# Optimization experiments

Hardware: AMD Instinct MI355X
Metric: run time of the kernel (lower is better)

Reference implementation:

```python
import jax, jax.numpy as jnp
import numpy as np
import math

B, P = 64, 2048
E_DRUG, E_PATH = 512, 512
ATTN_DIM, H, DEPTH = 1024, 8, 1
HD = ATTN_DIM // (2 * H)          # head_dim = 64
SCALING = HD ** (-0.5)
LAMBDA_INIT = 0.8 - 0.6 * math.exp(-0.3 * DEPTH)
EPS_SM = 1e-20
EPS_RMS = 1e-5


def stable_softmax(x, eps=EPS_SM):
    x = x.astype(jnp.float32)
    x = x - jnp.max(x, axis=-1, keepdims=True)
    ex = jnp.exp(x)
    return ex / (jnp.sum(ex, axis=-1, keepdims=True) + eps)


def setup_inputs() -> dict:
    key = jax.random.key(0)
    ks = jax.random.split(key, 11)
    d = 2 * H * HD  # = ATTN_DIM
    return {
        "query": jax.random.normal(ks[0], (B, 1, E_DRUG), jnp.float32),
        "key": jax.random.normal(ks[1], (B, P, E_PATH), jnp.float32),
        # Linear weights stored [in, out] (transpose of torch storage; same math)
        "Wq": jax.random.normal(ks[2], (E_DRUG, d), jnp.float32) * 0.02,
        "Wk": jax.random.normal(ks[3], (E_PATH, d), jnp.float32) * 0.02,
        "Wv": jax.random.normal(ks[4], (E_PATH, d), jnp.float32) * 0.02,
        "Wo": jax.random.normal(ks[5], (d, E_DRUG), jnp.float32) * 0.02,
        "lambda_q1": jax.random.normal(ks[6], (HD,), jnp.float32) * 0.1,
        "lambda_k1": jax.random.normal(ks[7], (HD,), jnp.float32) * 0.1,
        "lambda_q2": jax.random.normal(ks[8], (HD,), jnp.float32) * 0.1,
        "lambda_k2": jax.random.normal(ks[9], (HD,), jnp.float32) * 0.1,
        "rms_weight": jnp.ones((2 * HD,), jnp.float32),
    }


def reference(query, key, Wq, Wk, Wv, Wo,
              lambda_q1, lambda_k1, lambda_q2, lambda_k2, rms_weight):
    # Q: [B,1,H,2,HD] -> [B,H,2,1,HD]; K,V: [B,P,H,2,HD] -> [B,H,2,P,HD]
    Q = (query @ Wq).reshape(B, 1, H, 2, HD).transpose(0, 2, 3, 1, 4) * SCALING
    K = (key @ Wk).reshape(B, P, H, 2, HD).transpose(0, 2, 3, 1, 4)
    V = (key @ Wv).reshape(B, P, H, 2, HD)

    # scores: [B,H,2,1,P]
    scores = jnp.einsum('bhsqd,bhskd->bhsqk', Q, K)
    scores = stable_softmax(scores)

    lam1 = jnp.exp(jnp.sum(lambda_q1 * lambda_k1))
    lam2 = jnp.exp(jnp.sum(lambda_q2 * lambda_k2))
    lam = lam1 - lam2 + LAMBDA_INIT

    diff_attn = scores[:, :, 0] - lam * scores[:, :, 1]  # [B,H,1,P]

    V_cat = V.transpose(0, 2, 1, 3, 4).reshape(B, H, P, 2 * HD)  # [B,H,P,2HD]
    out = jnp.einsum('bhqp,bhpd->bhqd', diff_attn, V_cat)        # [B,H,1,2HD]

    # RMSNorm over last dim, affine
    var = jnp.mean(out * out, axis=-1, keepdims=True)
    out = out * jax.lax.rsqrt(var + EPS_RMS) * rms_weight
    out = out * (1.0 - LAMBDA_INIT)

    out = out.transpose(0, 2, 1, 3).reshape(B, 1, 2 * H * HD)
    out = out @ Wo  # [B,1,E_DRUG]
    return out, diff_attn
```

## Files before the change

### kernel.cpp

```cpp
#include <hip/hip_runtime.h>
#include <hip/hip_bf16.h>
#include <math.h>

#define B_ 64
#define P_ 2048
#define E_ 512
#define H_ 8
#define D_ 1024
#define NCH_ 16
#define NSC_ 64
#define NG_ 4
#define SMEM_FUSED (131072 + 4608 + 1280 + 64 + 64)

#define BAR() do { asm volatile("s_waitcnt lgkmcnt(0)" ::: "memory"); \
                   __builtin_amdgcn_s_barrier(); } while (0)
#define VM0() asm volatile("s_waitcnt vmcnt(0)" ::: "memory")

static constexpr float SCALING_C = 0.125f;
static constexpr float LAMBDA_INIT_C = 0.35550906759096966f;

typedef float f32x4 __attribute__((ext_vector_type(4)));
typedef float f32x2 __attribute__((ext_vector_type(2)));
typedef short bf16x8 __attribute__((ext_vector_type(8)));

static __device__ __forceinline__ short f2bf(float f) {
    unsigned u = __builtin_bit_cast(unsigned, f);
    unsigned r = (u + 0x7fffu + ((u >> 16) & 1u)) >> 16;
    return (short)r;
}

static __device__ __forceinline__ void gload_lds16(const float* g, char* l) {
    __builtin_amdgcn_global_load_lds(
        (const __attribute__((address_space(1))) void*)g,
        (__attribute__((address_space(3))) void*)l, 16, 0, 0);
}

__global__ __launch_bounds__(256) void k_qproj(const float* __restrict__ query,
                                               const float* __restrict__ Wq,
                                               const float* __restrict__ Wk,
                                               unsigned short* __restrict__ qkfrag) {
    int x = blockIdx.x, b = blockIdx.y, t = threadIdx.x;
    __shared__ float q[E_];
    __shared__ float qh[256];
    q[t] = query[b * E_ + t];
    q[t + 256] = query[b * E_ + t + 256];
    __syncthreads();
    {
        int j = x * 256 + t;
        const float* w = Wq + j;
        float s[8] = {0.f,0.f,0.f,0.f,0.f,0.f,0.f,0.f};
        #pragma unroll 4
        for (int e = 0; e < E_; e += 8) {
            #pragma unroll
            for (int k = 0; k < 8; ++k) s[k] += q[e + k] * w[(long)(e + k) * D_];
        }
        qh[t] = (((s[0]+s[1])+(s[2]+s[3])) + ((s[4]+s[5])+(s[6]+s[7]))) * SCALING_C;
    }
    __syncthreads();
    int hs_loc = t >> 6, l = t & 63;
    int hs = x * 4 + hs_loc;
    int e0 = l * 8;
    const float* qp = qh + hs_loc * 64;
    float acc[8];
    #pragma unroll
    for (int jj = 0; jj < 8; ++jj) {
        const f32x4* w = (const f32x4*)(Wk + (long)(e0 + jj) * D_ + hs * 64);
        float s = 0.f;
        #pragma unroll
        for (int d4 = 0; d4 < 16; ++d4) {
            f32x4 wv = w[d4];
            s += qp[d4 * 4 + 0] * wv[0] + qp[d4 * 4 + 1] * wv[1]
               + qp[d4 * 4 + 2] * wv[2] + qp[d4 * 4 + 3] * wv[3];
        }
        acc[jj] = s;
    }
    bf16x8 v;
    #pragma unroll
    for (int jj = 0; jj < 8; ++jj) v[jj] = f2bf(acc[jj]);
    *(bf16x8*)(qkfrag + (((long)b * 16 + (l >> 2)) * 64 + (l & 3) * 16 + hs) * 8) = v;
}

__global__ __launch_bounds__(512, 1) void k_fusedp(const float* __restrict__ key,
                                                   const unsigned short* __restrict__ qkfrag,
                                                   float* __restrict__ wexp,
                                                   float* __restrict__ ms, float* __restrict__ zs,
                                                   float* __restrict__ apart) {
    extern __shared__ __align__(16) char smem[];
    float* scr           = (float*)(smem + 131072);
    unsigned short* wbf  = (unsigned short*)(smem + 135680);
    float* fac_l         = (float*)(smem + 136960);
    float* mrun_l        = (float*)(smem + 137024);

    int pcg = blockIdx.x, b = blockIdx.y;
    int t = threadIdx.x, wv = t >> 6, l = t & 63;
    int pw = wv;
    int cw = wv - 4;
    int rt = cw >> 1, eh = cw & 1;
    int prow = rt * 16 + (l & 15);

    if (t < 16) mrun_l[t] = -3.0e38f;

#define P_ISSUE(cc) do {                                                          \
    char* bufc_ = smem + ((cc) & 1) * 65536;                                      \
    const float* gb_ = key + ((long)b * P_ + pcg * (NCH_ * 32) + (cc) * 32) * E_; \
    _Pragma("unroll")                                                             \
    for (int k_ = 0; k_ < 16; ++k_) {                                             \
        int row_ = pw * 8 + (k_ >> 1);                                            \
        int h_ = k_ & 1;                                                          \
        const float* g_ = gb_ + (long)row_ * E_ + (((h_ * 64 + l) ^ (row_ & 7)) << 2); \
        gload_lds16(g_, bufc_ + row_ * 2048 + h_ * 1024);                         \
    }                                                                             \
} while (0)

    bf16x8 qfr[8];
    f32x4 accp[8];
    if (wv >= 4) {
        const bf16x8* qf = (const bf16x8*)(qkfrag + (long)b * 16 * 64 * 8);
        #pragma unroll
        for (int s = 0; s < 8; ++s) qfr[s] = qf[(eh * 8 + s) * 64 + l];
        #pragma unroll
        for (int i = 0; i < 8; ++i) accp[i] = {0.f, 0.f, 0.f, 0.f};
    } else {
        P_ISSUE(0);
        VM0();
    }
    BAR();

    for (int c = 0; c < NCH_; ++c) {
        const char* bufc = smem + (c & 1) * 65536;
        if (wv < 4) {
            if (c < NCH_ - 1) P_ISSUE(c + 1);
        } else {
            f32x4 acc = {0.f, 0.f, 0.f, 0.f};
            const char* rbase = bufc + prow * 2048;
            int swz = prow & 7;
            #pragma unroll
            for (int s = 0; s < 8; ++s) {
                int e8 = eh * 256 + (l >> 4) * 8 + s * 32;
                int blk = (e8 >> 2) ^ swz;
                f32x4 xa = *(const f32x4*)(rbase + blk * 16);
                f32x4 xb = *(const f32x4*)(rbase + (blk ^ 1) * 16);
                bf16x8 a;
                a[0] = f2bf(xa[0]); a[1] = f2bf(xa[1]); a[2] = f2bf(xa[2]); a[3] = f2bf(xa[3]);
                a[4] = f2bf(xb[0]); a[5] = f2bf(xb[1]); a[6] = f2bf(xb[2]); a[7] = f2bf(xb[3]);
                acc = __builtin_amdgcn_mfma_f32_16x16x32_bf16(a, qfr[s], acc, 0, 0, 0);
            }
            #pragma unroll
            for (int r = 0; r < 4; ++r)
                scr[eh * 576 + (l & 15) * 36 + rt * 16 + (l >> 4) * 4 + r] = acc[r];
        }
        BAR();

        if (wv >= 4) {
            int hs = cw * 4 + (l >> 4);
            int i = l & 15;
            const float* s0p = scr + hs * 36 + i * 2;
            const float* s1p = s0p + 576;
            float v0 = s0p[0] + s1p[0];
            float v1 = s0p[1] + s1p[1];
            float m = fmaxf(v0, v1);
            #pragma unroll
            for (int o = 8; o > 0; o >>= 1) m = fmaxf(m, __shfl_xor(m, o));
            float e0v = expf(v0 - m), e1v = expf(v1 - m);
            float z = e0v + e1v;
            #pragma unroll
            for (int o = 8; o > 0; o >>= 1) z += __shfl_xor(z, o);
            float mold = mrun_l[hs];
            float mnew = fmaxf(mold, m);
            float wsc = expf(m - mnew);
            if (i == 0) {
                mrun_l[hs] = mnew;
                fac_l[hs] = expf(mold - mnew);
                ms[((long)(pcg * NCH_ + c) * B_ + b) * 16 + hs] = m;
                zs[((long)(pcg * NCH_ + c) * B_ + b) * 16 + hs] = z;
            }
            f32x2 wv2; wv2[0] = e0v; wv2[1] = e1v;
            *(f32x2*)(wexp + ((long)b * 16 + hs) * P_ + pcg * (NCH_ * 32) + c * 32 + i * 2) = wv2;
            unsigned lo = (unsigned short)f2bf(e0v * wsc);
            unsigned hi2 = (unsigned short)f2bf(e1v * wsc);
            *(unsigned*)(wbf + hs * 40 + i * 2) = lo | (hi2 << 16);
        }
        BAR();

        if (wv < 4) {
            VM0();
        } else {
            f32x4 frv;
            frv[0] = fac_l[(l >> 4) * 4 + 0];
            frv[1] = fac_l[(l >> 4) * 4 + 1];
            frv[2] = fac_l[(l >> 4) * 4 + 2];
            frv[3] = fac_l[(l >> 4) * 4 + 3];
            const unsigned short* wrow = wbf + (l & 15) * 40;
            int pbase = (l >> 4) * 8;
            bf16x8 af = *(const bf16x8*)(wrow + pbase);
            #pragma unroll
            for (int tile = 0; tile < 8; ++tile) {
                int e = cw * 128 + tile * 16 + (l & 15);
                bf16x8 bfv;
                #pragma unroll
                for (int j = 0; j < 8; ++j) {
                    const float* kf = (const float*)(bufc + (pbase + j) * 2048
                                       + (((e >> 2) ^ j) * 16) + ((e & 3) << 2));
                    bfv[j] = f2bf(*kf);
                }
                accp[tile] = accp[tile] * frv;
                accp[tile] = __builtin_amdgcn_mfma_f32_16x16x32_bf16(af, bfv, accp[tile], 0, 0, 0);
            }
        }
        BAR();
    }

    if (wv >= 4) {
        long abase = ((long)pcg * B_ + b) * 16 * E_;
        #pragma unroll
        for (int tile = 0; tile < 8; ++tile) {
            int e = cw * 128 + tile * 16 + (l & 15);
            #pragma unroll
            for (int r = 0; r < 4; ++r)
                apart[abase + (long)((l >> 4) * 4 + r) * E_ + e] = accp[tile][r];
        }
    }
#undef P_ISSUE
}

__global__ __launch_bounds__(256) void k_comb(const float* __restrict__ wexp,
                                              const float* __restrict__ ms, const float* __restrict__ zs,
                                              const float* __restrict__ apart,
                                              const float* __restrict__ lq1, const float* __restrict__ lk1,
                                              const float* __restrict__ lq2, const float* __restrict__ lk2,
                                              const float* __restrict__ Wv, const float* __restrict__ rmsw,
                                              float* __restrict__ out1, float* __restrict__ on) {
    int h = blockIdx.x, b = blockIdx.y, t = threadIdx.x;
    __shared__ float lam_s;
    __shared__ float mc0s[NSC_], mc1s[NSC_], zc0s[NSC_], zc1s[NSC_];
    __shared__ float c0s[NSC_], c1s[NSC_];
    __shared__ float attk[E_];
    __shared__ float onred[2][128];
    __shared__ float red[4];
    int hs0 = 2 * h, hs1 = 2 * h + 1;
    if (t < 64) {
        float v1 = lq1[t] * lk1[t];
        float v2 = lq2[t] * lk2[t];
        #pragma unroll
        for (int o = 32; o > 0; o >>= 1) { v1 += __shfl_xor(v1, o); v2 += __shfl_xor(v2, o); }
        if (t == 0) lam_s = expf(v1) - expf(v2) + LAMBDA_INIT_C;
    }
    if (t >= 64 && t < 64 + NSC_) {
        int c = t - 64;
        mc0s[c] = ms[((long)c * B_ + b) * 16 + hs0];
        mc1s[c] = ms[((long)c * B_ + b) * 16 + hs1];
        zc0s[c] = zs[((long)c * B_ + b) * 16 + hs0];
        zc1s[c] = zs[((long)c * B_ + b) * 16 + hs1];
    }
    __syncthreads();
    float m0 = -3.0e38f, m1 = -3.0e38f;
    #pragma unroll 8
    for (int c = 0; c < NSC_; ++c) { m0 = fmaxf(m0, mc0s[c]); m1 = fmaxf(m1, mc1s[c]); }
    float z0 = 0.f, z1 = 0.f;
    #pragma unroll 8
    for (int c = 0; c < NSC_; ++c) {
        z0 += zc0s[c] * expf(mc0s[c] - m0);
        z1 += zc1s[c] * expf(mc1s[c] - m1);
    }
    float lam = lam_s;
    float i0 = 1.f / (z0 + 1e-20f);
    float i1 = lam / (z1 + 1e-20f);
    if (t < NSC_) {
        c0s[t] = expf(mc0s[t] - m0) * i0;
        c1s[t] = expf(mc1s[t] - m1) * i1;
    }
    __syncthreads();
    const float* w0p = wexp + ((long)b * 16 + hs0) * P_;
    const float* w1p = wexp + ((long)b * 16 + hs1) * P_;
    float* dst = out1 + ((long)b * H_ + h) * P_;
    #pragma unroll
    for (int c8 = 0; c8 < 8; ++c8) {
        int p = c8 * 256 + t;
        dst[p] = w0p[p] * c0s[p >> 5] - w1p[p] * c1s[p >> 5];
    }
    float cg0[NG_], cg1[NG_];
    #pragma unroll
    for (int g = 0; g < NG_; ++g) {
        float mg0 = -3.0e38f, mg1 = -3.0e38f;
        #pragma unroll
        for (int q = 0; q < NCH_; ++q) {
            mg0 = fmaxf(mg0, mc0s[g * NCH_ + q]);
            mg1 = fmaxf(mg1, mc1s[g * NCH_ + q]);
        }
        cg0[g] = expf(mg0 - m0) * i0;
        cg1[g] = expf(mg1 - m1) * i1;
    }
    #pragma unroll
    for (int k = 0; k < 2; ++k) {
        int e = k * 256 + t;
        float s = 0.f;
        #pragma unroll
        for (int g = 0; g < NG_; ++g) {
            s += cg0[g] * apart[(((long)g * B_ + b) * 16 + hs0) * E_ + e]
               - cg1[g] * apart[(((long)g * B_ + b) * 16 + hs1) * E_ + e];
        }
        attk[e] = s;
    }
    __syncthreads();
    int j = t & 127, half = t >> 7;
    const float* w = Wv + (long)(half * 256) * D_ + h * 128 + j;
    const float* aa = attk + half * 256;
    float s[8] = {0.f,0.f,0.f,0.f,0.f,0.f,0.f,0.f};
    #pragma unroll 4
    for (int e = 0; e < 256; e += 8) {
        #pragma unroll
        for (int k = 0; k < 8; ++k) s[k] += aa[e + k] * w[(long)(e + k) * D_];
    }
    onred[half][j] = ((s[0]+s[1])+(s[2]+s[3])) + ((s[4]+s[5])+(s[6]+s[7]));
    __syncthreads();
    float v = 0.f;
    if (t < 128) v = onred[0][t] + onred[1][t];
    float sq = v * v;
    int wv2 = t >> 6, ln = t & 63;
    #pragma unroll
    for (int o = 32; o > 0; o >>= 1) sq += __shfl_xor(sq, o);
    if (ln == 0) red[wv2] = sq;
    __syncthreads();
    float tot = red[0] + red[1];
    float scale = rsqrtf(tot * (1.f / 128.f) + 1e-5f) * (1.f - LAMBDA_INIT_C);
    if (t < 128) on[(long)b * D_ + h * 128 + t] = v * scale * rmsw[t];
}

__global__ __launch_bounds__(256) void k_wo(const float* __restrict__ on,
                                            const float* __restrict__ Wo,
                                            float* __restrict__ wop) {
    int kc = blockIdx.x >> 1, oc = blockIdx.x & 1, b = blockIdx.y;
    int t = threadIdx.x;
    __shared__ float sh[256];
    sh[t] = on[(long)b * D_ + kc * 256 + t];
    __syncthreads();
    int o = oc * 256 + t;
    const float* w = Wo + (long)(kc * 256) * 512 + o;
    float s[8] = {0.f,0.f,0.f,0.f,0.f,0.f,0.f,0.f};
    #pragma unroll 4
    for (int k = 0; k < 256; k += 8) {
        #pragma unroll
        for (int q = 0; q < 8; ++q) s[q] += sh[k + q] * w[(long)(k + q) * 512];
    }
    wop[((long)kc * B_ + b) * 512 + o] = ((s[0]+s[1])+(s[2]+s[3])) + ((s[4]+s[5])+(s[6]+s[7]));
}

__global__ __launch_bounds__(256) void k_wored(const float* __restrict__ wop,
                                               float* __restrict__ out0) {
    int b = blockIdx.x, t = threadIdx.x;
    #pragma unroll
    for (int i = 0; i < 2; ++i) {
        int o = i * 256 + t;
        float s = 0.f;
        #pragma unroll
        for (int kc = 0; kc < 4; ++kc) s += wop[((long)kc * B_ + b) * 512 + o];
        out0[(long)b * 512 + o] = s;
    }
}

extern "C" void kernel_launch(void* const* d_in, const int* in_sizes, int n_in,
                              void* d_out, int out_size, void* d_ws, size_t ws_size,
                              hipStream_t stream) {
    const float* query = (const float*)d_in[0];
    const float* key   = (const float*)d_in[1];
    const float* Wq    = (const float*)d_in[2];
    const float* Wk    = (const float*)d_in[3];
    const float* Wv    = (const float*)d_in[4];
    const float* Wo    = (const float*)d_in[5];
    const float* lq1   = (const float*)d_in[6];
    const float* lk1   = (const float*)d_in[7];
    const float* lq2   = (const float*)d_in[8];
    const float* lk2   = (const float*)d_in[9];
    const float* rmsw  = (const float*)d_in[10];

    float* out0 = (float*)d_out;
    float* out1 = out0 + B_ * E_;

    unsigned short* qkfrag = (unsigned short*)d_ws;
    float* wexp  = (float*)d_ws + 262144;
    float* apart = wexp + (long)B_ * 16 * P_;
    float* ms    = apart + (long)NG_ * B_ * 16 * E_;
    float* zs    = ms + NSC_ * B_ * 16;
    float* on    = zs + NSC_ * B_ * 16;
    float* wop   = on + B_ * D_;

    hipFuncSetAttribute((const void*)k_fusedp,
                        hipFuncAttributeMaxDynamicSharedMemorySize, SMEM_FUSED);

    hipLaunchKernelGGL(k_qproj,  dim3(4, B_),   dim3(256), 0, stream, query, Wq, Wk, qkfrag);
    hipLaunchKernelGGL(k_fusedp, dim3(NG_, B_), dim3(512), SMEM_FUSED, stream,
                       key, qkfrag, wexp, ms, zs, apart);
    hipLaunchKernelGGL(k_comb,   dim3(H_, B_),  dim3(256), 0, stream, wexp, ms, zs, apart,
                       lq1, lk1, lq2, lk2, Wv, rmsw, out1, on);
    hipLaunchKernelGGL(k_wo,     dim3(8, B_),   dim3(256), 0, stream, on, Wo, wop);
    hipLaunchKernelGGL(k_wored,  dim3(B_),      dim3(256), 0, stream, wop, out0);
}
```

Before: 125.8 us.

## Replace producer/consumer wave split with uniform waves and 4-deep load pipeline

Drops the split where four waves only load key rows and four waves compute. All eight waves now issue async global-to-LDS loads for 16-row chunks into a 4-slot ring buffer, three chunks ahead, and share the QK score and PV MFMA work, with each wave owning a 64-column slice of E. Chunks shrink from 32 to 16 rows, so the block runs twice as many chunk iterations and barriers and writes twice as many per-chunk max/sum partials, which the combine kernel now indexes by 16-row chunk. Half of each PV MFMA's K dimension is zero-padded, which wastes tensor throughput.

```diff
diff --git a/kernel.cpp b/kernel.cpp
--- a/kernel.cpp
+++ b/kernel.cpp
@@ -7,14 +7,13 @@
 #define E_ 512
 #define H_ 8
 #define D_ 1024
-#define NCH_ 16
-#define NSC_ 64
+#define NCH_ 32
+#define NSC_ 128
 #define NG_ 4
-#define SMEM_FUSED (131072 + 4608 + 1280 + 64 + 64)
+#define SMEM_FUSED (131072 + 10240 + 1536 + 64 + 64)
 
 #define BAR() do { asm volatile("s_waitcnt lgkmcnt(0)" ::: "memory"); \
                    __builtin_amdgcn_s_barrier(); } while (0)
-#define VM0() asm volatile("s_waitcnt vmcnt(0)" ::: "memory")
 
 static constexpr float SCALING_C = 0.125f;
 static constexpr float LAMBDA_INIT_C = 0.35550906759096966f;
@@ -87,56 +86,57 @@
                                                    float* __restrict__ apart) {
     extern __shared__ __align__(16) char smem[];
     float* scr           = (float*)(smem + 131072);
-    unsigned short* wbf  = (unsigned short*)(smem + 135680);
-    float* fac_l         = (float*)(smem + 136960);
-    float* mrun_l        = (float*)(smem + 137024);
+    unsigned short* wbf  = (unsigned short*)(smem + 141312);
+    float* fac_l         = (float*)(smem + 142848);
+    float* mrun_l        = (float*)(smem + 142912);
 
     int pcg = blockIdx.x, b = blockIdx.y;
-    int t = threadIdx.x, wv = t >> 6, l = t & 63;
-    int pw = wv;
-    int cw = wv - 4;
-    int rt = cw >> 1, eh = cw & 1;
-    int prow = rt * 16 + (l & 15);
+    int t = threadIdx.x, w = t >> 6, l = t & 63;
+    int prow = l & 15;
 
     if (t < 16) mrun_l[t] = -3.0e38f;
-
-#define P_ISSUE(cc) do {                                                          \
-    char* bufc_ = smem + ((cc) & 1) * 65536;                                      \
-    const float* gb_ = key + ((long)b * P_ + pcg * (NCH_ * 32) + (cc) * 32) * E_; \
-    _Pragma("unroll")                                                             \
-    for (int k_ = 0; k_ < 16; ++k_) {                                             \
-        int row_ = pw * 8 + (k_ >> 1);                                            \
-        int h_ = k_ & 1;                                                          \
-        const float* g_ = gb_ + (long)row_ * E_ + (((h_ * 64 + l) ^ (row_ & 7)) << 2); \
-        gload_lds16(g_, bufc_ + row_ * 2048 + h_ * 1024);                         \
-    }                                                                             \
+    if (t < 256) wbf[(t >> 4) * 48 + 16 + (t & 15)] = 0;
+
+    bf16x8 qfr[2];
+    {
+        const bf16x8* qf = (const bf16x8*)(qkfrag + (long)b * 16 * 64 * 8);
+        qfr[0] = qf[(2 * w) * 64 + l];
+        qfr[1] = qf[(2 * w + 1) * 64 + l];
+    }
+
+    const float* gb = key + ((long)b * P_ + pcg * (NCH_ * 16)) * E_;
+
+#define ISSUE(cc) do {                                                          \
+    char* bufd_ = smem + ((cc) & 3) * 32768;                                    \
+    const float* gsrc_ = gb + (long)(cc) * 16 * E_;                             \
+    _Pragma("unroll")                                                           \
+    for (int k_ = 0; k_ < 4; ++k_) {                                            \
+        int row_ = 2 * w + (k_ >> 1);                                           \
+        int h_ = k_ & 1;                                                        \
+        gload_lds16(gsrc_ + (long)row_ * E_ + (((h_ * 64 + l) ^ (row_ & 7)) << 2), \
+                    bufd_ + row_ * 2048 + h_ * 1024);                           \
+    }                                                                           \
 } while (0)
 
-    bf16x8 qfr[8];
-    f32x4 accp[8];
-    if (wv >= 4) {
-        const bf16x8* qf = (const bf16x8*)(qkfrag + (long)b * 16 * 64 * 8);
-        #pragma unroll
-        for (int s = 0; s < 8; ++s) qfr[s] = qf[(eh * 8 + s) * 64 + l];
-        #pragma unroll
-        for (int i = 0; i < 8; ++i) accp[i] = {0.f, 0.f, 0.f, 0.f};
-    } else {
-        P_ISSUE(0);
-        VM0();
-    }
+    ISSUE(0); ISSUE(1); ISSUE(2);
+    asm volatile("s_waitcnt vmcnt(8)" ::: "memory");
     BAR();
 
+    f32x4 accp[4];
+    #pragma unroll
+    for (int i = 0; i < 4; ++i) accp[i] = {0.f, 0.f, 0.f, 0.f};
+
     for (int c = 0; c < NCH_; ++c) {
-        const char* bufc = smem + (c & 1) * 65536;
-        if (wv < 4) {
-            if (c < NCH_ - 1) P_ISSUE(c + 1);
-        } else {
-            f32x4 acc = {0.f, 0.f, 0.f, 0.f};
+        const char* bufc = smem + (c & 3) * 32768;
+        if (c + 3 < NCH_) ISSUE(c + 3);
+
+        {
             const char* rbase = bufc + prow * 2048;
             int swz = prow & 7;
-            #pragma unroll
-            for (int s = 0; s < 8; ++s) {
-                int e8 = eh * 256 + (l >> 4) * 8 + s * 32;
+            f32x4 acc = {0.f, 0.f, 0.f, 0.f};
+            #pragma unroll
+            for (int s = 0; s < 2; ++s) {
+                int e8 = w * 64 + (l >> 4) * 8 + s * 32;
                 int blk = (e8 >> 2) ^ swz;
                 f32x4 xa = *(const f32x4*)(rbase + blk * 16);
                 f32x4 xb = *(const f32x4*)(rbase + (blk ^ 1) * 16);
@@ -147,80 +147,82 @@
             }
             #pragma unroll
             for (int r = 0; r < 4; ++r)
-                scr[eh * 576 + (l & 15) * 36 + rt * 16 + (l >> 4) * 4 + r] = acc[r];
+                scr[w * 320 + (l & 15) * 20 + (l >> 4) * 4 + r] = acc[r];
         }
         BAR();
 
-        if (wv >= 4) {
-            int hs = cw * 4 + (l >> 4);
-            int i = l & 15;
-            const float* s0p = scr + hs * 36 + i * 2;
-            const float* s1p = s0p + 576;
-            float v0 = s0p[0] + s1p[0];
-            float v1 = s0p[1] + s1p[1];
-            float m = fmaxf(v0, v1);
+        if (t < 256) {
+            int hs = t >> 4, i = t & 15;
+            float v = 0.f;
+            #pragma unroll
+            for (int eh = 0; eh < 8; ++eh) v += scr[eh * 320 + hs * 20 + i];
+            float m = v;
             #pragma unroll
             for (int o = 8; o > 0; o >>= 1) m = fmaxf(m, __shfl_xor(m, o));
-            float e0v = expf(v0 - m), e1v = expf(v1 - m);
-            float z = e0v + e1v;
+            float ev = expf(v - m);
+            float z = ev;
             #pragma unroll
             for (int o = 8; o > 0; o >>= 1) z += __shfl_xor(z, o);
             float mold = mrun_l[hs];
             float mnew = fmaxf(mold, m);
-            float wsc = expf(m - mnew);
             if (i == 0) {
                 mrun_l[hs] = mnew;
                 fac_l[hs] = expf(mold - mnew);
                 ms[((long)(pcg * NCH_ + c) * B_ + b) * 16 + hs] = m;
                 zs[((long)(pcg * NCH_ + c) * B_ + b) * 16 + hs] = z;
             }
-            f32x2 wv2; wv2[0] = e0v; wv2[1] = e1v;
-            *(f32x2*)(wexp + ((long)b * 16 + hs) * P_ + pcg * (NCH_ * 32) + c * 32 + i * 2) = wv2;
-            unsigned lo = (unsigned short)f2bf(e0v * wsc);
-            unsigned hi2 = (unsigned short)f2bf(e1v * wsc);
-            *(unsigned*)(wbf + hs * 40 + i * 2) = lo | (hi2 << 16);
+            wexp[((long)b * 16 + hs) * P_ + pcg * (NCH_ * 16) + c * 16 + i] = ev;
+            wbf[hs * 48 + i] = (unsigned short)f2bf(ev * expf(m - mnew));
         }
         BAR();
 
-        if (wv < 4) {
-            VM0();
-        } else {
+        {
             f32x4 frv;
             frv[0] = fac_l[(l >> 4) * 4 + 0];
             frv[1] = fac_l[(l >> 4) * 4 + 1];
             frv[2] = fac_l[(l >> 4) * 4 + 2];
             frv[3] = fac_l[(l >> 4) * 4 + 3];
-            const unsigned short* wrow = wbf + (l & 15) * 40;
+            const unsigned short* wrow = wbf + (l & 15) * 48;
             int pbase = (l >> 4) * 8;
             bf16x8 af = *(const bf16x8*)(wrow + pbase);
-            #pragma unroll
-            for (int tile = 0; tile < 8; ++tile) {
-                int e = cw * 128 + tile * 16 + (l & 15);
+            bool act = pbase < 16;
+            #pragma unroll
+            for (int tile = 0; tile < 4; ++tile) {
+                int e = w * 64 + tile * 16 + (l & 15);
                 bf16x8 bfv;
-                #pragma unroll
-                for (int j = 0; j < 8; ++j) {
-                    const float* kf = (const float*)(bufc + (pbase + j) * 2048
-                                       + (((e >> 2) ^ j) * 16) + ((e & 3) << 2));
-                    bfv[j] = f2bf(*kf);
+                if (act) {
+                    #pragma unroll
+                    for (int j = 0; j < 8; ++j) {
+                        int rr = pbase + j;
+                        const float* kf = (const float*)(bufc + rr * 2048
+                                           + (((e >> 2) ^ (rr & 7)) * 16) + ((e & 3) << 2));
+                        bfv[j] = f2bf(*kf);
+                    }
+                } else {
+                    #pragma unroll
+                    for (int j = 0; j < 8; ++j) bfv[j] = 0;
                 }
                 accp[tile] = accp[tile] * frv;
                 accp[tile] = __builtin_amdgcn_mfma_f32_16x16x32_bf16(af, bfv, accp[tile], 0, 0, 0);
             }
         }
+        if (c < NCH_ - 3)       asm volatile("s_waitcnt vmcnt(8)" ::: "memory");
+        else if (c == NCH_ - 3) asm volatile("s_waitcnt vmcnt(4)" ::: "memory");
+        else if (c == NCH_ - 2) asm volatile("s_waitcnt vmcnt(0)" ::: "memory");
         BAR();
     }
 
-    if (wv >= 4) {
+    {
         long abase = ((long)pcg * B_ + b) * 16 * E_;
         #pragma unroll
-        for (int tile = 0; tile < 8; ++tile) {
-            int e = cw * 128 + tile * 16 + (l & 15);
+        for (int tile = 0; tile < 4; ++tile) {
+            int e = w * 64 + tile * 16 + (l & 15);
             #pragma unroll
             for (int r = 0; r < 4; ++r)
                 apart[abase + (long)((l >> 4) * 4 + r) * E_ + e] = accp[tile][r];
         }
     }
-#undef P_ISSUE
+#undef ISSUE
 }
 
 __global__ __launch_bounds__(256) void k_comb(const float* __restrict__ wexp,
@@ -276,13 +278,13 @@
     #pragma unroll
     for (int c8 = 0; c8 < 8; ++c8) {
         int p = c8 * 256 + t;
-        dst[p] = w0p[p] * c0s[p >> 5] - w1p[p] * c1s[p >> 5];
+        dst[p] = w0p[p] * c0s[p >> 4] - w1p[p] * c1s[p >> 4];
     }
     float cg0[NG_], cg1[NG_];
     #pragma unroll
     for (int g = 0; g < NG_; ++g) {
         float mg0 = -3.0e38f, mg1 = -3.0e38f;
-        #pragma unroll
+        #pragma unroll 8
         for (int q = 0; q < NCH_; ++q) {
             mg0 = fmaxf(mg0, mc0s[g * NCH_ + q]);
             mg1 = fmaxf(mg1, mc1s[g * NCH_ + q]);
```

Result: slower. 155.1 us (+23.3%).
